# Performance work log

Measured on AMD Instinct MI355X. Metric: run time of the kernel, lower is better.

Reference implementation:

```python
import jax, jax.numpy as jnp
import numpy as np

N = 50000          # nodes
E = 800000         # edges
H = 64             # hidden_dim == node_embedding_dim (heads=1)
ED = 32            # edge_embedding_dim
L = 3              # num_layers - 1 TransformerConv layers
G = 256            # graphs in batch
NODE_CAT = 42
EDGE_CAT = 10
OUT = 32
SCALE = 1.0 / np.sqrt(H)


def segment_softmax(logits, seg, num_segments):
    mx = jax.ops.segment_max(logits, seg, num_segments=num_segments)
    e = jnp.exp(logits - mx[seg])
    denom = jax.ops.segment_sum(e, seg, num_segments=num_segments)
    return e / denom[seg]


def setup_inputs() -> dict:
    key = jax.random.key(0)
    ks = jax.random.split(key, 16)

    def init(k, shape, fan_in):
        return (jax.random.normal(k, shape, jnp.float32) / np.sqrt(fan_in))

    inp = {}
    inp["x"] = jax.random.randint(ks[0], (N,), 0, NODE_CAT)
    inp["edge_index"] = jax.random.randint(ks[1], (2, E), 0, N)
    inp["edge_attr"] = jax.random.randint(ks[2], (E,), 0, EDGE_CAT)
    inp["batch"] = jnp.sort(jax.random.randint(ks[3], (N,), 0, G))

    inp["node_emb"] = init(ks[4], (NODE_CAT, H), 1)
    inp["edge_emb"] = init(ks[5], (EDGE_CAT, ED), 1)
    # stacked per-layer TransformerConv params (input dim is H for all layers
    # since node_embedding_dim == hidden_dim)
    inp["Wq"] = init(ks[6], (L, H, H), H)
    inp["Wk"] = init(ks[7], (L, H, H), H)
    inp["Wv"] = init(ks[8], (L, H, H), H)
    inp["We"] = init(ks[9], (L, ED, H), ED)   # lin_edge, bias=False in PyG
    inp["Wskip"] = init(ks[10], (L, H, H), H)
    inp["bq"] = jnp.zeros((L, H), jnp.float32)
    inp["bk"] = jnp.zeros((L, H), jnp.float32)
    inp["bv"] = jnp.zeros((L, H), jnp.float32)
    inp["bskip"] = jnp.zeros((L, H), jnp.float32)
    # attentional aggregation readout
    inp["gate_W"] = init(ks[11], (H, 1), H)
    inp["gate_b"] = jnp.zeros((1,), jnp.float32)
    inp["out_W"] = init(ks[12], (H, OUT), H)
    inp["out_b"] = jnp.zeros((OUT,), jnp.float32)
    return inp


def reference(x, edge_index, edge_attr, batch, node_emb, edge_emb,
              Wq, Wk, Wv, We, Wskip, bq, bk, bv, bskip,
              gate_W, gate_b, out_W, out_b):
    src, dst = edge_index[0], edge_index[1]
    h = node_emb[x]            # [N, H] node embedding lookup
    e_feat = edge_emb[edge_attr]  # [E, ED] edge embedding lookup

    for l in range(L):
        q = h @ Wq[l] + bq[l]          # [N, H]
        k = h @ Wk[l] + bk[l]
        v = h @ Wv[l] + bv[l]
        e = e_feat @ We[l]             # [E, H]
        k_j = k[src] + e               # key_j += lin_edge(edge_attr)
        alpha = jnp.sum(q[dst] * k_j, axis=-1) * SCALE   # [E]
        a = segment_softmax(alpha, dst, N)               # softmax over dst nbhd
        msg = (v[src] + e) * a[:, None]                  # [E, H]
        agg = jax.ops.segment_sum(msg, dst, num_segments=N)
        h = jax.nn.relu(agg + h @ Wskip[l] + bskip[l])   # root/skip + ReLU

    # AttentionalAggregation: gate = gate_nn(x); x = nn(x); softmax gate per graph
    gate = (h @ gate_W + gate_b)[:, 0]   # [N]
    y = h @ out_W + out_b                # [N, OUT]
    g = segment_softmax(gate, batch, G)  # [N]
    return jax.ops.segment_sum(g[:, None] * y, batch, num_segments=G)  # [G, OUT]
```

## Files before the change

### kernel.cpp

```cpp
#include <hip/hip_runtime.h>
#include <hip/hip_bf16.h>

#define N_NODES 50000
#define N_EDGES 800000
#define H 64
#define ED 32
#define LAYERS 3
#define NGRAPH 256
#define OUTD 32
#define SCALE 0.125f

#define BNODES 128
#define NBUCK 391
#define NB_HISTB 256
#define EPB (N_EDGES / NB_HISTB)

#define FB_HIST 256
#define FB_TE   8
#define FB_GB   2
#define FB_WB   192
#define FB_TAB  42
#define NB_FRONT (FB_HIST + FB_TE + FB_GB + FB_WB + FB_TAB)

#define NB_GATHER 3125
#define NB_SCAN   98
#define NB_AGG    3125

typedef __attribute__((ext_vector_type(8))) short bf16x8;
typedef __attribute__((ext_vector_type(4))) float f32x4;
typedef unsigned short ushort_t;

__device__ __forceinline__ unsigned f2bf(float f) {
    unsigned u = __float_as_uint(f);
    return (u + 0x7FFFu + ((u >> 16) & 1u)) >> 16;
}

__device__ __forceinline__ float radd16(float x) {
    x += __int_as_float(__builtin_amdgcn_update_dpp(0, __float_as_int(x), 0xB1, 0xF, 0xF, true));
    x += __int_as_float(__builtin_amdgcn_update_dpp(0, __float_as_int(x), 0x4E, 0xF, 0xF, true));
    x += __int_as_float(__builtin_amdgcn_update_dpp(0, __float_as_int(x), 0x124, 0xF, 0xF, true));
    x += __int_as_float(__builtin_amdgcn_update_dpp(0, __float_as_int(x), 0x128, 0xF, 0xF, true));
    return x;
}

__device__ __forceinline__ void build_bstart(const int* __restrict__ tot,
                                             int* bst, int* part, int t) {
    int u0 = t * 2, u1 = t * 2 + 1;
    int a0 = (u0 < NBUCK) ? tot[u0] : 0;
    int a1 = (u1 < NBUCK) ? tot[u1] : 0;
    part[t] = a0 + a1;
    __syncthreads();
    for (int off = 1; off < 256; off <<= 1) {
        int add = (t >= off) ? part[t - off] : 0;
        __syncthreads();
        part[t] += add;
        __syncthreads();
    }
    int excl = part[t] - (a0 + a1);
    if (u0 < NBUCK) bst[u0] = excl;
    if (u1 < NBUCK) bst[u1] = excl + a0;
    if (t == 0) bst[NBUCK] = N_EDGES;
    __syncthreads();
}

__global__ __launch_bounds__(256) void k_front(
    const int* __restrict__ x, const float* __restrict__ node_emb,
    const float* __restrict__ edge_emb, const float* __restrict__ We, float* __restrict__ te,
    const int* __restrict__ ei, int* __restrict__ hist,
    const int* __restrict__ batch, int* __restrict__ gs,
    const float* __restrict__ Wq, const float* __restrict__ Wk,
    const float* __restrict__ Wv, const float* __restrict__ Wsk,
    const float* __restrict__ bq, const float* __restrict__ bk,
    const float* __restrict__ bv, const float* __restrict__ bsk,
    ushort_t* __restrict__ wb16,
    unsigned* __restrict__ tqs, unsigned* __restrict__ tkv)
{
    __shared__ int lh[NBUCK];
    __shared__ float tb[4][64];
    int b = blockIdx.x, t = threadIdx.x;
    if (b < FB_HIST) {
        for (int i = t; i < NBUCK; i += 256) lh[i] = 0;
        __syncthreads();
        const int* dstp = ei + N_EDGES + b * EPB;
        for (int i = t; i < EPB; i += 256)
            atomicAdd(&lh[dstp[i] >> 7], 1);
        __syncthreads();
        for (int i = t; i < NBUCK; i += 256) hist[i * NB_HISTB + b] = lh[i];
    } else if (b < FB_HIST + FB_TE) {
        int i = (b - FB_HIST) * 256 + t;
        if (i < LAYERS * 10 * H) {
            int c = i & 63;
            int cat = (i >> 6) % 10;
            int l = i / (10 * H);
            float acc = 0.f;
            for (int d = 0; d < ED; d++)
                acc += edge_emb[cat * ED + d] * We[((size_t)l * ED + d) * H + c];
            te[i] = acc;
        }
    } else if (b < FB_HIST + FB_TE + FB_GB) {
        int g = (b - FB_HIST - FB_TE) * 256 + t;
        if (g <= NGRAPH) {
            int lo = 0, hi = N_NODES;
            while (lo < hi) {
                int mid = (lo + hi) >> 1;
                if (batch[mid] < g) lo = mid + 1; else hi = mid;
            }
            gs[g] = lo;
        }
    } else if (b < FB_HIST + FB_TE + FB_GB + FB_WB) {
        int g = (b - FB_HIST - FB_TE - FB_GB) * 256 + t;
        int l = g >> 14;
        int rem = g & 16383;
        int c_id = rem >> 11;
        int rr = (rem >> 3) & 255;
        int j = rem & 7;
        int mat = rr >> 6, n = rr & 63;
        int k = ((c_id >> 2) << 5) + ((c_id & 3) << 3) + j;
        const float* Wm = (mat == 0) ? Wq : (mat == 1) ? Wk : (mat == 2) ? Wv : Wsk;
        wb16[g] = (ushort_t)f2bf(Wm[(size_t)l * 4096 + k * 64 + n]);
    } else {
        int cat = b - (FB_HIST + FB_TE + FB_GB + FB_WB);
        int mat = t >> 6, c = t & 63;
        const float* Wm = (mat == 0) ? Wq : (mat == 1) ? Wk : (mat == 2) ? Wv : Wsk;
        const float* bm = (mat == 0) ? bq : (mat == 1) ? bk : (mat == 2) ? bv : bsk;
        float acc = bm[c];
        for (int k = 0; k < H; k++)
            acc += node_emb[cat * H + k] * Wm[k * 64 + c];
        tb[mat][c] = acc;
        __syncthreads();
        if (t < 64) {
            tqs[cat * 64 + t] = f2bf(tb[0][t]) | (f2bf(tb[3][t]) << 16);
            tkv[cat * 64 + t] = f2bf(tb[2][t]) | (f2bf(tb[1][t]) << 16);
        }
    }
}

__global__ __launch_bounds__(256) void k_scan_gather(
    const int* __restrict__ x,
    const unsigned* __restrict__ tqs, const unsigned* __restrict__ tkv,
    unsigned* __restrict__ qs_out, unsigned* __restrict__ kv_out,
    int* __restrict__ hist, int* __restrict__ tot)
{
    __shared__ int sv[256];
    int b = blockIdx.x, t = threadIdx.x;
    if (b < NB_GATHER) {
        int idx = b * 256 + t;
        int n = idx >> 4, c4 = idx & 15;
        int cat = x[n];
        ((uint4*)qs_out)[idx] = ((const uint4*)tqs)[cat * 16 + c4];
        ((uint4*)kv_out)[idx] = ((const uint4*)tkv)[cat * 16 + c4];
    } else {
        int sb = b - NB_GATHER;
        for (int r = 0; r < 4; r++) {
            int u = sb * 4 + r;
            if (u < NBUCK) {
                int v = hist[u * NB_HISTB + t];
                sv[t] = v;
                __syncthreads();
                for (int off = 1; off < 256; off <<= 1) {
                    int add = (t >= off) ? sv[t - off] : 0;
                    __syncthreads();
                    sv[t] += add;
                    __syncthreads();
                }
                int incl = sv[t];
                hist[u * NB_HISTB + t] = incl - v;
                if (t == 255) tot[u] = incl;
                __syncthreads();
            }
        }
    }
}

__global__ __launch_bounds__(256) void k_scatter(
    const int* __restrict__ ei, const int* __restrict__ ea,
    const int* __restrict__ hist, const int* __restrict__ tot,
    int* __restrict__ pmid)
{
    __shared__ int bst[NBUCK + 1];
    __shared__ int part[256];
    __shared__ int curS[NBUCK];
    int b = blockIdx.x, t = threadIdx.x;
    build_bstart(tot, bst, part, t);
    for (int u = t; u < NBUCK; u += 256)
        curS[u] = bst[u] + hist[u * NB_HISTB + b];
    __syncthreads();
    int e0 = b * EPB;
    for (int i = t; i < EPB; i += 256) {
        int e = e0 + i;
        int src = ei[e], dst = ei[N_EDGES + e], cat = ea[e];
        int pos = atomicAdd(&curS[dst >> 7], 1);
        pmid[pos] = src | (cat << 16) | ((dst & 127) << 20);
    }
}

__global__ __launch_bounds__(256) void k_final(
    const int* __restrict__ pmid, const int* __restrict__ tot,
    int* __restrict__ packed, int* __restrict__ row_start, int* __restrict__ row_end)
{
    __shared__ int bst[NBUCK + 1];
    __shared__ int part[256];
    __shared__ int cnt[BNODES];
    __shared__ int scan_s[BNODES];
    int b = blockIdx.x, t = threadIdx.x;
    build_bstart(tot, bst, part, t);
    int beg = bst[b], end = bst[b + 1];
    if (t < BNODES) cnt[t] = 0;
    __syncthreads();
    for (int e = beg + t; e < end; e += 256)
        atomicAdd(&cnt[(pmid[e] >> 20) & 127], 1);
    __syncthreads();
    if (t < BNODES) scan_s[t] = cnt[t];
    __syncthreads();
    for (int off = 1; off < BNODES; off <<= 1) {
        int add = (t >= off && t < BNODES) ? scan_s[t - off] : 0;
        __syncthreads();
        if (t < BNODES) scan_s[t] += add;
        __syncthreads();
    }
    if (t < BNODES) {
        int c = cnt[t];
        int excl = scan_s[t] - c;
        int node = b * BNODES + t;
        if (node < N_NODES) {
            row_start[node] = beg + excl;
            row_end[node] = beg + excl + c;
        }
        cnt[t] = beg + excl;
    }
    __syncthreads();
    for (int e = beg + t; e < end; e += 256) {
        int p = pmid[e];
        int pos = atomicAdd(&cnt[(p >> 20) & 127], 1);
        packed[pos] = p & 0xFFFFF;
    }
}

struct EdgeLd { uint4 kv; float4 t; };
__device__ __forceinline__ EdgeLd edge_load(int pkt, const unsigned* __restrict__ kv32,
                                            const float* tel, int i16) {
    EdgeLd r;
    r.kv = *(const uint4*)(kv32 + ((size_t)(pkt & 0xFFFF) << 6) + (i16 << 2));
    r.t  = *(const float4*)(tel + ((pkt >> 16) << 6) + (i16 << 2));
    return r;
}
__device__ __forceinline__ float edge_dot(const EdgeLd& e, const float4& q4) {
    float p;
    p = (__uint_as_float(e.kv.x & 0xFFFF0000u) + e.t.x) * q4.x;
    p = fmaf(__uint_as_float(e.kv.y & 0xFFFF0000u) + e.t.y, q4.y, p);
    p = fmaf(__uint_as_float(e.kv.z & 0xFFFF0000u) + e.t.z, q4.z, p);
    p = fmaf(__uint_as_float(e.kv.w & 0xFFFF0000u) + e.t.w, q4.w, p);
    return radd16(p) * SCALE;
}
__device__ __forceinline__ float4 edge_val(const EdgeLd& e) {
    float4 v;
    v.x = __uint_as_float(e.kv.x << 16) + e.t.x;
    v.y = __uint_as_float(e.kv.y << 16) + e.t.y;
    v.z = __uint_as_float(e.kv.z << 16) + e.t.z;
    v.w = __uint_as_float(e.kv.w << 16) + e.t.w;
    return v;
}

__global__ __launch_bounds__(256, 4) void k_agg(
    const int* __restrict__ row_start, const int* __restrict__ row_end,
    const int* __restrict__ packed,
    const unsigned* __restrict__ qs_in, const unsigned* __restrict__ kv_in,
    const float* __restrict__ te,
    const ushort_t* __restrict__ wbn, const float* __restrict__ bqn,
    const float* __restrict__ bkn, const float* __restrict__ bvn,
    const float* __restrict__ bsn,
    unsigned* __restrict__ qs_out, unsigned* __restrict__ kv_out,
    float* __restrict__ hf, const float* __restrict__ gW,
    const float* __restrict__ gb, float* __restrict__ gate)
{
    __shared__ float tel[10 * 64];
    __shared__ ushort_t hs16[16 * 64];
    int t = threadIdx.x;
    int wave = t >> 6, lane = t & 63;
    int g = lane >> 4, i16 = lane & 15;
    int dst = blockIdx.x * 16 + wave * 4 + g;
    int beg = row_start[dst];
    int end = row_end[dst];
    uint4 uq = *(const uint4*)(qs_in + (size_t)dst * 64 + (i16 << 2));
    for (int i = t; i < 10 * 64; i += 256) tel[i] = te[i];
    __syncthreads();
    float4 q4, s4;
    q4.x = __uint_as_float(uq.x << 16); s4.x = __uint_as_float(uq.x & 0xFFFF0000u);
    q4.y = __uint_as_float(uq.y << 16); s4.y = __uint_as_float(uq.y & 0xFFFF0000u);
    q4.z = __uint_as_float(uq.z << 16); s4.z = __uint_as_float(uq.z & 0xFFFF0000u);
    q4.w = __uint_as_float(uq.w << 16); s4.w = __uint_as_float(uq.w & 0xFFFF0000u);
    float m = -1e30f, l = 0.f;
    float4 acc = {0.f, 0.f, 0.f, 0.f};
    int e = beg;
    for (; e + 3 < end; e += 4) {
        int p0 = packed[e], p1 = packed[e + 1], p2 = packed[e + 2], p3 = packed[e + 3];
        EdgeLd e0 = edge_load(p0, kv_in, tel, i16);
        EdgeLd e1 = edge_load(p1, kv_in, tel, i16);
        EdgeLd e2 = edge_load(p2, kv_in, tel, i16);
        EdgeLd e3 = edge_load(p3, kv_in, tel, i16);
        float a0 = edge_dot(e0, q4), a1 = edge_dot(e1, q4);
        float a2 = edge_dot(e2, q4), a3 = edge_dot(e3, q4);
        float mn = fmaxf(m, fmaxf(fmaxf(a0, a1), fmaxf(a2, a3)));
        float corr = __expf(m - mn);
        float w0 = __expf(a0 - mn), w1 = __expf(a1 - mn);
        float w2 = __expf(a2 - mn), w3 = __expf(a3 - mn);
        float4 v0 = edge_val(e0), v1 = edge_val(e1), v2 = edge_val(e2), v3 = edge_val(e3);
        acc.x = fmaf(w0, v0.x, fmaf(w1, v1.x, fmaf(w2, v2.x, fmaf(w3, v3.x, acc.x * corr))));
        acc.y = fmaf(w0, v0.y, fmaf(w1, v1.y, fmaf(w2, v2.y, fmaf(w3, v3.y, acc.y * corr))));
        acc.z = fmaf(w0, v0.z, fmaf(w1, v1.z, fmaf(w2, v2.z, fmaf(w3, v3.z, acc.z * corr))));
        acc.w = fmaf(w0, v0.w, fmaf(w1, v1.w, fmaf(w2, v2.w, fmaf(w3, v3.w, acc.w * corr))));
        l = fmaf(l, corr, (w0 + w1) + (w2 + w3));
        m = mn;
    }
    for (; e < end; e++) {
        int pkt = packed[e];
        EdgeLd e0 = edge_load(pkt, kv_in, tel, i16);
        float a = edge_dot(e0, q4);
        float mn = fmaxf(m, a);
        float corr = __expf(m - mn);
        float w = __expf(a - mn);
        float4 v4 = edge_val(e0);
        acc.x = fmaf(w, v4.x, acc.x * corr);
        acc.y = fmaf(w, v4.y, acc.y * corr);
        acc.z = fmaf(w, v4.z, acc.z * corr);
        acc.w = fmaf(w, v4.w, acc.w * corr);
        l = fmaf(l, corr, w);
        m = mn;
    }
    float inv = (l > 0.f) ? 1.f / l : 0.f;
    float4 hv;
    hv.x = fmaxf(acc.x * inv + s4.x, 0.f);
    hv.y = fmaxf(acc.y * inv + s4.y, 0.f);
    hv.z = fmaxf(acc.z * inv + s4.z, 0.f);
    hv.w = fmaxf(acc.w * inv + s4.w, 0.f);
    if (hf) *(float4*)(hf + (size_t)dst * H + (i16 << 2)) = hv;
    if (gW) {
        float4 g4 = *(const float4*)(gW + (i16 << 2));
        float p = hv.x * g4.x + hv.y * g4.y + hv.z * g4.z + hv.w * g4.w;
        p = radd16(p);
        if (i16 == 0) gate[dst] = p + gb[0];
    }
    if (wbn) {
        uint2 hp;
        hp.x = f2bf(hv.x) | (f2bf(hv.y) << 16);
        hp.y = f2bf(hv.z) | (f2bf(hv.w) << 16);
        *(uint2*)(hs16 + (((wave * 4 + g) << 6) + (i16 << 2))) = hp;
        __syncthreads();
        int n16 = lane & 15, quad = lane >> 4;
        f32x4 oacc[4];
        #pragma unroll
        for (int i = 0; i < 4; i++) oacc[i] = (f32x4){0.f, 0.f, 0.f, 0.f};
        #pragma unroll
        for (int kb = 0; kb < 2; kb++) {
            bf16x8 afr = *(const bf16x8*)(hs16 + ((n16 << 6) + kb * 32 + quad * 8));
            #pragma unroll
            for (int mat = 0; mat < 4; mat++) {
                int ct = mat * 4 + wave;
                const bf16x8* bp = (const bf16x8*)(wbn + (((kb * 4 + quad) << 11) + ((ct * 16 + n16) << 3)));
                oacc[mat] = __builtin_amdgcn_mfma_f32_16x16x32_bf16(afr, *bp, oacc[mat], 0, 0, 0);
            }
        }
        int col = (wave << 4) + n16;
        float bQ = bqn[col], bK = bkn[col], bV = bvn[col], bS = bsn[col];
        int nb = blockIdx.x * 16 + quad * 4;
        #pragma unroll
        for (int r = 0; r < 4; r++) {
            qs_out[(size_t)(nb + r) * 64 + col] = f2bf(oacc[0][r] + bQ) | (f2bf(oacc[3][r] + bS) << 16);
            kv_out[(size_t)(nb + r) * 64 + col] = f2bf(oacc[2][r] + bV) | (f2bf(oacc[1][r] + bK) << 16);
        }
    }
}

__global__ __launch_bounds__(256) void k_readout2(
    const float* __restrict__ h, const float* __restrict__ oW,
    const float* __restrict__ ob, const float* __restrict__ gate,
    const int* __restrict__ gs, float* __restrict__ out)
{
    __shared__ float hs[8][H + 1];
    __shared__ float red[256];
    __shared__ float den_s[8];
    __shared__ float gmax_s, den_tot;
    int t = threadIdx.x;
    int g = blockIdx.x;
    int ln = t >> 5, o = t & 31;
    float wreg[H];
    #pragma unroll
    for (int i = 0; i < H; i++) wreg[i] = oW[i * OUTD + o];
    int beg = gs[g], end = gs[g + 1];
    float mx = -INFINITY;
    for (int n = beg + t; n < end; n += 256) mx = fmaxf(mx, gate[n]);
    red[t] = mx;
    __syncthreads();
    for (int sft = 128; sft > 0; sft >>= 1) {
        if (t < sft) red[t] = fmaxf(red[t], red[t + sft]);
        __syncthreads();
    }
    if (t == 0) gmax_s = red[0];
    __syncthreads();
    float gm = gmax_s;
    float acc = 0.f, den = 0.f;
    for (int n0 = beg; n0 < end; n0 += 8) {
        __syncthreads();
        for (int i = t; i < 8 * H; i += 256) {
            int r = i >> 6, c = i & 63;
            int n = n0 + r;
            hs[r][c] = (n < end) ? h[(size_t)n * H + c] : 0.f;
        }
        __syncthreads();
        int n = n0 + ln;
        if (n < end) {
            float wt = __expf(gate[n] - gm);
            float d0 = 0.f;
            #pragma unroll
            for (int i = 0; i < H; i++) d0 += hs[ln][i] * wreg[i];
            acc += wt * d0;
            if (o == 0) den += wt;
        }
    }
    __syncthreads();
    red[t] = acc;
    if (o == 0) den_s[ln] = den;
    __syncthreads();
    for (int sft = 4; sft >= 1; sft >>= 1) {
        if (ln < sft) red[t] += red[t + sft * 32];
        __syncthreads();
    }
    if (t == 0) {
        float dt = 0.f;
        #pragma unroll
        for (int i = 0; i < 8; i++) dt += den_s[i];
        den_tot = dt;
    }
    __syncthreads();
    if (ln == 0) {
        float dt = den_tot;
        out[g * OUTD + o] = (dt > 0.f) ? red[o] / dt + ob[o] : 0.f;
    }
}

extern "C" void kernel_launch(void* const* d_in, const int* in_sizes, int n_in,
                              void* d_out, int out_size, void* d_ws, size_t ws_size,
                              hipStream_t stream)
{
    const int* x        = (const int*)d_in[0];
    const int* ei       = (const int*)d_in[1];
    const int* ea       = (const int*)d_in[2];
    const int* batch    = (const int*)d_in[3];
    const float* node_emb = (const float*)d_in[4];
    const float* edge_emb = (const float*)d_in[5];
    const float* Wq    = (const float*)d_in[6];
    const float* Wk    = (const float*)d_in[7];
    const float* Wv    = (const float*)d_in[8];
    const float* We    = (const float*)d_in[9];
    const float* Wskip = (const float*)d_in[10];
    const float* bq    = (const float*)d_in[11];
    const float* bk    = (const float*)d_in[12];
    const float* bv    = (const float*)d_in[13];
    const float* bskip = (const float*)d_in[14];
    const float* gate_W = (const float*)d_in[15];
    const float* gate_b = (const float*)d_in[16];
    const float* out_W  = (const float*)d_in[17];
    const float* out_b  = (const float*)d_in[18];
    float* out = (float*)d_out;

    const size_t NH = (size_t)N_NODES * H;
    float* ws   = (float*)d_ws;
    unsigned* qs_a = (unsigned*)ws;
    unsigned* kv_a = qs_a + NH;
    unsigned* qs_b = kv_a + NH;
    unsigned* kv_b = qs_b + NH;
    float* hf32 = (float*)(kv_b + NH);
    float* te   = hf32 + NH;
    float* gate = te + LAYERS * 10 * H;
    int* row_start = (int*)(gate + N_NODES);
    int* row_end   = row_start + N_NODES;
    int* packed    = row_end + N_NODES;
    int* pmid      = packed + N_EDGES;
    int* hist      = pmid + N_EDGES;
    int* tot       = hist + NBUCK * NB_HISTB;
    int* gs        = tot + NBUCK;
    unsigned* tqs  = (unsigned*)(gs + NGRAPH + 1);
    unsigned* tkv  = tqs + FB_TAB * 64;
    ushort_t* wb16 = (ushort_t*)(tkv + FB_TAB * 64);

    k_front<<<NB_FRONT, 256, 0, stream>>>(x, node_emb, edge_emb, We, te, ei, hist, batch, gs,
                                          Wq, Wk, Wv, Wskip, bq, bk, bv, bskip, wb16, tqs, tkv);
    k_scan_gather<<<NB_GATHER + NB_SCAN, 256, 0, stream>>>(x, tqs, tkv, qs_a, kv_a, hist, tot);
    k_scatter<<<NB_HISTB, 256, 0, stream>>>(ei, ea, hist, tot, pmid);
    k_final<<<NBUCK, 256, 0, stream>>>(pmid, tot, packed, row_start, row_end);

    k_agg<<<NB_AGG, 256, 0, stream>>>(
        row_start, row_end, packed, qs_a, kv_a, te,
        wb16 + (size_t)1 * 16384, bq + H, bk + H, bv + H, bskip + H, qs_b, kv_b,
        nullptr, nullptr, nullptr, nullptr);
    k_agg<<<NB_AGG, 256, 0, stream>>>(
        row_start, row_end, packed, qs_b, kv_b, te + 10 * H,
        wb16 + (size_t)2 * 16384, bq + 2 * H, bk + 2 * H, bv + 2 * H, bskip + 2 * H, qs_a, kv_a,
        nullptr, nullptr, nullptr, nullptr);
    k_agg<<<NB_AGG, 256, 0, stream>>>(
        row_start, row_end, packed, qs_a, kv_a, te + 2 * 10 * H,
        nullptr, nullptr, nullptr, nullptr, nullptr, nullptr, nullptr,
        hf32, gate_W, gate_b, gate);

    k_readout2<<<NGRAPH, 256, 0, stream>>>(hf32, out_W, out_b, gate, gs, out);
}
```

Before: 269.9 us.

## Fuse layer-0 node gather into aggregation via per-category LDS tables and packed edge keys

Removes the separate layer-0 node-feature gather pass. The edge packet now encodes the combined source node category and edge category, so the first aggregation kernel reads the per-category key/value table from LDS instead of per-node global rows. All aggregation kernels also stage each block's edge packets into LDS when they fit, and the kernels are specialized by template mode to drop runtime null checks. The cost is an extra x[src] lookup in the scatter and more LDS per block in the first layer, which may reduce occupancy.

```diff
diff --git a/kernel.cpp b/kernel.cpp
--- a/kernel.cpp
+++ b/kernel.cpp
@@ -9,6 +9,7 @@
 #define NGRAPH 256
 #define OUTD 32
 #define SCALE 0.125f
+#define NCAT 42
 
 #define BNODES 128
 #define NBUCK 391
@@ -19,12 +20,12 @@
 #define FB_TE   8
 #define FB_GB   2
 #define FB_WB   192
-#define FB_TAB  42
+#define FB_TAB  NCAT
 #define NB_FRONT (FB_HIST + FB_TE + FB_GB + FB_WB + FB_TAB)
 
-#define NB_GATHER 3125
 #define NB_SCAN   98
 #define NB_AGG    3125
+#define PKCAP     768
 
 typedef __attribute__((ext_vector_type(8))) short bf16x8;
 typedef __attribute__((ext_vector_type(4))) float f32x4;
@@ -135,45 +136,32 @@
     }
 }
 
-__global__ __launch_bounds__(256) void k_scan_gather(
-    const int* __restrict__ x,
-    const unsigned* __restrict__ tqs, const unsigned* __restrict__ tkv,
-    unsigned* __restrict__ qs_out, unsigned* __restrict__ kv_out,
-    int* __restrict__ hist, int* __restrict__ tot)
+__global__ __launch_bounds__(256) void k_scan(int* __restrict__ hist, int* __restrict__ tot)
 {
     __shared__ int sv[256];
-    int b = blockIdx.x, t = threadIdx.x;
-    if (b < NB_GATHER) {
-        int idx = b * 256 + t;
-        int n = idx >> 4, c4 = idx & 15;
-        int cat = x[n];
-        ((uint4*)qs_out)[idx] = ((const uint4*)tqs)[cat * 16 + c4];
-        ((uint4*)kv_out)[idx] = ((const uint4*)tkv)[cat * 16 + c4];
-    } else {
-        int sb = b - NB_GATHER;
-        for (int r = 0; r < 4; r++) {
-            int u = sb * 4 + r;
-            if (u < NBUCK) {
-                int v = hist[u * NB_HISTB + t];
-                sv[t] = v;
+    int sb = blockIdx.x, t = threadIdx.x;
+    for (int r = 0; r < 4; r++) {
+        int u = sb * 4 + r;
+        if (u < NBUCK) {
+            int v = hist[u * NB_HISTB + t];
+            sv[t] = v;
+            __syncthreads();
+            for (int off = 1; off < 256; off <<= 1) {
+                int add = (t >= off) ? sv[t - off] : 0;
                 __syncthreads();
-                for (int off = 1; off < 256; off <<= 1) {
-                    int add = (t >= off) ? sv[t - off] : 0;
-                    __syncthreads();
-                    sv[t] += add;
-                    __syncthreads();
-                }
-                int incl = sv[t];
-                hist[u * NB_HISTB + t] = incl - v;
-                if (t == 255) tot[u] = incl;
+                sv[t] += add;
                 __syncthreads();
             }
+            int incl = sv[t];
+            hist[u * NB_HISTB + t] = incl - v;
+            if (t == 255) tot[u] = incl;
+            __syncthreads();
         }
     }
 }
 
 __global__ __launch_bounds__(256) void k_scatter(
-    const int* __restrict__ ei, const int* __restrict__ ea,
+    const int* __restrict__ ei, const int* __restrict__ ea, const int* __restrict__ x,
     const int* __restrict__ hist, const int* __restrict__ tot,
     int* __restrict__ pmid)
 {
@@ -189,8 +177,9 @@
     for (int i = t; i < EPB; i += 256) {
         int e = e0 + i;
         int src = ei[e], dst = ei[N_EDGES + e], cat = ea[e];
+        int xs = x[src];
         int pos = atomicAdd(&curS[dst >> 7], 1);
-        pmid[pos] = src | (cat << 16) | ((dst & 127) << 20);
+        pmid[pos] = src | ((cat * NCAT + xs) << 16) | ((dst & 127) << 25);
     }
 }
 
@@ -208,7 +197,7 @@
     if (t < BNODES) cnt[t] = 0;
     __syncthreads();
     for (int e = beg + t; e < end; e += 256)
-        atomicAdd(&cnt[(pmid[e] >> 20) & 127], 1);
+        atomicAdd(&cnt[((unsigned)pmid[e] >> 25) & 127], 1);
     __syncthreads();
     if (t < BNODES) scan_s[t] = cnt[t];
     __syncthreads();
@@ -231,19 +220,12 @@
     __syncthreads();
     for (int e = beg + t; e < end; e += 256) {
         int p = pmid[e];
-        int pos = atomicAdd(&cnt[(p >> 20) & 127], 1);
-        packed[pos] = p & 0xFFFFF;
+        int pos = atomicAdd(&cnt[((unsigned)p >> 25) & 127], 1);
+        packed[pos] = p & 0x1FFFFFF;
     }
 }
 
 struct EdgeLd { uint4 kv; float4 t; };
-__device__ __forceinline__ EdgeLd edge_load(int pkt, const unsigned* __restrict__ kv32,
-                                            const float* tel, int i16) {
-    EdgeLd r;
-    r.kv = *(const uint4*)(kv32 + ((size_t)(pkt & 0xFFFF) << 6) + (i16 << 2));
-    r.t  = *(const float4*)(tel + ((pkt >> 16) << 6) + (i16 << 2));
-    return r;
-}
 __device__ __forceinline__ float edge_dot(const EdgeLd& e, const float4& q4) {
     float p;
     p = (__uint_as_float(e.kv.x & 0xFFFF0000u) + e.t.x) * q4.x;
@@ -261,29 +243,42 @@
     return v;
 }
 
-__global__ __launch_bounds__(256, 4) void k_agg(
+template<int MODE>
+__device__ __forceinline__ void agg_body(
     const int* __restrict__ row_start, const int* __restrict__ row_end,
-    const int* __restrict__ packed,
+    const int* __restrict__ packed, const int* __restrict__ x,
     const unsigned* __restrict__ qs_in, const unsigned* __restrict__ kv_in,
+    const unsigned* __restrict__ tqs, const unsigned* __restrict__ tkv,
     const float* __restrict__ te,
     const ushort_t* __restrict__ wbn, const float* __restrict__ bqn,
     const float* __restrict__ bkn, const float* __restrict__ bvn,
     const float* __restrict__ bsn,
     unsigned* __restrict__ qs_out, unsigned* __restrict__ kv_out,
     float* __restrict__ hf, const float* __restrict__ gW,
-    const float* __restrict__ gb, float* __restrict__ gate)
-{
-    __shared__ float tel[10 * 64];
-    __shared__ ushort_t hs16[16 * 64];
-    int t = threadIdx.x;
+    const float* __restrict__ gb, float* __restrict__ gate,
+    float* tel, unsigned* tqsl, unsigned* tkvl, ushort_t* hs16, int* pkl)
+{
+    int t = threadIdx.x, bid = blockIdx.x;
     int wave = t >> 6, lane = t & 63;
     int g = lane >> 4, i16 = lane & 15;
-    int dst = blockIdx.x * 16 + wave * 4 + g;
-    int beg = row_start[dst];
-    int end = row_end[dst];
-    uint4 uq = *(const uint4*)(qs_in + (size_t)dst * 64 + (i16 << 2));
-    for (int i = t; i < 10 * 64; i += 256) tel[i] = te[i];
-    __syncthreads();
+    int dst = bid * 16 + wave * 4 + g;
+    int beg = row_start[dst], end = row_end[dst];
+    int beg0 = row_start[bid * 16];
+    int cnt = row_end[bid * 16 + 15] - beg0;
+    bool use_lds = (cnt <= PKCAP);
+    for (int i = t; i < 640; i += 256) tel[i] = te[i];
+    if constexpr (MODE == 0) {
+        for (int i = t; i < NCAT * 64; i += 256) { tqsl[i] = tqs[i]; tkvl[i] = tkv[i]; }
+    }
+    if (use_lds) for (int i = t; i < cnt; i += 256) pkl[i] = packed[beg0 + i];
+    uint4 uq = {0u, 0u, 0u, 0u};
+    if constexpr (MODE != 0)
+        uq = *(const uint4*)(qs_in + (size_t)dst * 64 + (i16 << 2));
+    __syncthreads();
+    if constexpr (MODE == 0) {
+        int xd = x[dst];
+        uq = *(const uint4*)(tqsl + (xd << 6) + (i16 << 2));
+    }
     float4 q4, s4;
     q4.x = __uint_as_float(uq.x << 16); s4.x = __uint_as_float(uq.x & 0xFFFF0000u);
     q4.y = __uint_as_float(uq.y << 16); s4.y = __uint_as_float(uq.y & 0xFFFF0000u);
@@ -291,56 +286,71 @@
     q4.w = __uint_as_float(uq.w << 16); s4.w = __uint_as_float(uq.w & 0xFFFF0000u);
     float m = -1e30f, l = 0.f;
     float4 acc = {0.f, 0.f, 0.f, 0.f};
-    int e = beg;
-    for (; e + 3 < end; e += 4) {
-        int p0 = packed[e], p1 = packed[e + 1], p2 = packed[e + 2], p3 = packed[e + 3];
-        EdgeLd e0 = edge_load(p0, kv_in, tel, i16);
-        EdgeLd e1 = edge_load(p1, kv_in, tel, i16);
-        EdgeLd e2 = edge_load(p2, kv_in, tel, i16);
-        EdgeLd e3 = edge_load(p3, kv_in, tel, i16);
-        float a0 = edge_dot(e0, q4), a1 = edge_dot(e1, q4);
-        float a2 = edge_dot(e2, q4), a3 = edge_dot(e3, q4);
-        float mn = fmaxf(m, fmaxf(fmaxf(a0, a1), fmaxf(a2, a3)));
-        float corr = __expf(m - mn);
-        float w0 = __expf(a0 - mn), w1 = __expf(a1 - mn);
-        float w2 = __expf(a2 - mn), w3 = __expf(a3 - mn);
-        float4 v0 = edge_val(e0), v1 = edge_val(e1), v2 = edge_val(e2), v3 = edge_val(e3);
-        acc.x = fmaf(w0, v0.x, fmaf(w1, v1.x, fmaf(w2, v2.x, fmaf(w3, v3.x, acc.x * corr))));
-        acc.y = fmaf(w0, v0.y, fmaf(w1, v1.y, fmaf(w2, v2.y, fmaf(w3, v3.y, acc.y * corr))));
-        acc.z = fmaf(w0, v0.z, fmaf(w1, v1.z, fmaf(w2, v2.z, fmaf(w3, v3.z, acc.z * corr))));
-        acc.w = fmaf(w0, v0.w, fmaf(w1, v1.w, fmaf(w2, v2.w, fmaf(w3, v3.w, acc.w * corr))));
-        l = fmaf(l, corr, (w0 + w1) + (w2 + w3));
-        m = mn;
-    }
-    for (; e < end; e++) {
-        int pkt = packed[e];
-        EdgeLd e0 = edge_load(pkt, kv_in, tel, i16);
-        float a = edge_dot(e0, q4);
-        float mn = fmaxf(m, a);
-        float corr = __expf(m - mn);
-        float w = __expf(a - mn);
-        float4 v4 = edge_val(e0);
-        acc.x = fmaf(w, v4.x, acc.x * corr);
-        acc.y = fmaf(w, v4.y, acc.y * corr);
-        acc.z = fmaf(w, v4.z, acc.z * corr);
-        acc.w = fmaf(w, v4.w, acc.w * corr);
-        l = fmaf(l, corr, w);
-        m = mn;
-    }
+
+    auto eload = [&](int pkt) {
+        EdgeLd r;
+        unsigned catx = ((unsigned)pkt >> 16) & 0x1FFu;
+        int cat = (int)((catx * 1561u) >> 16);
+        r.t = *(const float4*)(tel + (cat << 6) + (i16 << 2));
+        if constexpr (MODE == 0) {
+            int xc = (int)catx - cat * NCAT;
+            r.kv = *(const uint4*)(tkvl + (xc << 6) + (i16 << 2));
+        } else {
+            int src = pkt & 0xFFFF;
+            r.kv = *(const uint4*)(kv_in + ((size_t)src << 6) + (i16 << 2));
+        }
+        return r;
+    };
+    auto run = [&](auto PKT) {
+        int e = beg;
+        for (; e + 3 < end; e += 4) {
+            int p0 = PKT(e), p1 = PKT(e + 1), p2 = PKT(e + 2), p3 = PKT(e + 3);
+            EdgeLd e0 = eload(p0), e1 = eload(p1), e2 = eload(p2), e3 = eload(p3);
+            float a0 = edge_dot(e0, q4), a1 = edge_dot(e1, q4);
+            float a2 = edge_dot(e2, q4), a3 = edge_dot(e3, q4);
+            float mn = fmaxf(m, fmaxf(fmaxf(a0, a1), fmaxf(a2, a3)));
+            float corr = __expf(m - mn);
+            float w0 = __expf(a0 - mn), w1 = __expf(a1 - mn);
+            float w2 = __expf(a2 - mn), w3 = __expf(a3 - mn);
+            float4 v0 = edge_val(e0), v1 = edge_val(e1), v2 = edge_val(e2), v3 = edge_val(e3);
+            acc.x = fmaf(w0, v0.x, fmaf(w1, v1.x, fmaf(w2, v2.x, fmaf(w3, v3.x, acc.x * corr))));
+            acc.y = fmaf(w0, v0.y, fmaf(w1, v1.y, fmaf(w2, v2.y, fmaf(w3, v3.y, acc.y * corr))));
+            acc.z = fmaf(w0, v0.z, fmaf(w1, v1.z, fmaf(w2, v2.z, fmaf(w3, v3.z, acc.z * corr))));
+            acc.w = fmaf(w0, v0.w, fmaf(w1, v1.w, fmaf(w2, v2.w, fmaf(w3, v3.w, acc.w * corr))));
+            l = fmaf(l, corr, (w0 + w1) + (w2 + w3));
+            m = mn;
+        }
+        for (; e < end; e++) {
+            EdgeLd e0 = eload(PKT(e));
+            float a = edge_dot(e0, q4);
+            float mn = fmaxf(m, a);
+            float corr = __expf(m - mn);
+            float w = __expf(a - mn);
+            float4 v4 = edge_val(e0);
+            acc.x = fmaf(w, v4.x, acc.x * corr);
+            acc.y = fmaf(w, v4.y, acc.y * corr);
+            acc.z = fmaf(w, v4.z, acc.z * corr);
+            acc.w = fmaf(w, v4.w, acc.w * corr);
+            l = fmaf(l, corr, w);
+            m = mn;
+        }
+    };
+    if (use_lds) run([&](int e) { return pkl[e - beg0]; });
+    else         run([&](int e) { return packed[e]; });
+
     float inv = (l > 0.f) ? 1.f / l : 0.f;
     float4 hv;
     hv.x = fmaxf(acc.x * inv + s4.x, 0.f);
     hv.y = fmaxf(acc.y * inv + s4.y, 0.f);
     hv.z = fmaxf(acc.z * inv + s4.z, 0.f);
     hv.w = fmaxf(acc.w * inv + s4.w, 0.f);
-    if (hf) *(float4*)(hf + (size_t)dst * H + (i16 << 2)) = hv;
-    if (gW) {
+    if constexpr (MODE == 2) {
+        *(float4*)(hf + (size_t)dst * H + (i16 << 2)) = hv;
         float4 g4 = *(const float4*)(gW + (i16 << 2));
         float p = hv.x * g4.x + hv.y * g4.y + hv.z * g4.z + hv.w * g4.w;
         p = radd16(p);
         if (i16 == 0) gate[dst] = p + gb[0];
-    }
-    if (wbn) {
+    } else {
         uint2 hp;
         hp.x = f2bf(hv.x) | (f2bf(hv.y) << 16);
         hp.y = f2bf(hv.z) | (f2bf(hv.w) << 16);
@@ -362,13 +372,66 @@
         }
         int col = (wave << 4) + n16;
         float bQ = bqn[col], bK = bkn[col], bV = bvn[col], bS = bsn[col];
-        int nb = blockIdx.x * 16 + quad * 4;
+        int nb = bid * 16 + quad * 4;
         #pragma unroll
         for (int r = 0; r < 4; r++) {
             qs_out[(size_t)(nb + r) * 64 + col] = f2bf(oacc[0][r] + bQ) | (f2bf(oacc[3][r] + bS) << 16);
             kv_out[(size_t)(nb + r) * 64 + col] = f2bf(oacc[2][r] + bV) | (f2bf(oacc[1][r] + bK) << 16);
         }
     }
+}
+
+__global__ __launch_bounds__(256, 4) void k_agg0(
+    const int* __restrict__ row_start, const int* __restrict__ row_end,
+    const int* __restrict__ packed, const int* __restrict__ x,
+    const unsigned* __restrict__ tqs, const unsigned* __restrict__ tkv,
+    const float* __restrict__ te,
+    const ushort_t* __restrict__ wbn, const float* __restrict__ bqn,
+    const float* __restrict__ bkn, const float* __restrict__ bvn,
+    const float* __restrict__ bsn,
+    unsigned* __restrict__ qs_out, unsigned* __restrict__ kv_out)
+{
+    __shared__ float tel[640];
+    __shared__ unsigned tqsl[NCAT * 64];
+    __shared__ unsigned tkvl[NCAT * 64];
+    __shared__ ushort_t hs16[1024];
+    __shared__ int pkl[PKCAP];
+    agg_body<0>(row_start, row_end, packed, x, nullptr, nullptr, tqs, tkv, te,
+                wbn, bqn, bkn, bvn, bsn, qs_out, kv_out,
+                nullptr, nullptr, nullptr, nullptr, tel, tqsl, tkvl, hs16, pkl);
+}
+
+__global__ __launch_bounds__(256, 4) void k_agg1(
+    const int* __restrict__ row_start, const int* __restrict__ row_end,
+    const int* __restrict__ packed,
+    const unsigned* __restrict__ qs_in, const unsigned* __restrict__ kv_in,
+    const float* __restrict__ te,
+    const ushort_t* __restrict__ wbn, const float* __restrict__ bqn,
+    const float* __restrict__ bkn, const float* __restrict__ bvn,
+    const float* __restrict__ bsn,
+    unsigned* __restrict__ qs_out, unsigned* __restrict__ kv_out)
+{
+    __shared__ float tel[640];
+    __shared__ ushort_t hs16[1024];
+    __shared__ int pkl[PKCAP];
+    agg_body<1>(row_start, row_end, packed, nullptr, qs_in, kv_in, nullptr, nullptr, te,
+                wbn, bqn, bkn, bvn, bsn, qs_out, kv_out,
+                nullptr, nullptr, nullptr, nullptr, tel, nullptr, nullptr, hs16, pkl);
+}
+
+__global__ __launch_bounds__(256, 4) void k_agg2(
+    const int* __restrict__ row_start, const int* __restrict__ row_end,
+    const int* __restrict__ packed,
+    const unsigned* __restrict__ qs_in, const unsigned* __restrict__ kv_in,
+    const float* __restrict__ te,
+    float* __restrict__ hf, const float* __restrict__ gW,
+    const float* __restrict__ gb, float* __restrict__ gate)
+{
+    __shared__ float tel[640];
+    __shared__ int pkl[PKCAP];
+    agg_body<2>(row_start, row_end, packed, nullptr, qs_in, kv_in, nullptr, nullptr, te,
+                nullptr, nullptr, nullptr, nullptr, nullptr, nullptr, nullptr,
+                hf, gW, gb, gate, tel, nullptr, nullptr, nullptr, pkl);
 }
 
 __global__ __launch_bounds__(256) void k_readout2(
@@ -485,21 +548,18 @@
 
     k_front<<<NB_FRONT, 256, 0, stream>>>(x, node_emb, edge_emb, We, te, ei, hist, batch, gs,
                                           Wq, Wk, Wv, Wskip, bq, bk, bv, bskip, wb16, tqs, tkv);
-    k_scan_gather<<<NB_GATHER + NB_SCAN, 256, 0, stream>>>(x, tqs, tkv, qs_a, kv_a, hist, tot);
-    k_scatter<<<NB_HISTB, 256, 0, stream>>>(ei, ea, hist, tot, pmid);
+    k_scan<<<NB_SCAN, 256, 0, stream>>>(hist, tot);
+    k_scatter<<<NB_HISTB, 256, 0, stream>>>(ei, ea, x, hist, tot, pmid);
     k_final<<<NBUCK, 256, 0, stream>>>(pmid, tot, packed, row_start, row_end);
 
-    k_agg<<<NB_AGG, 256, 0, stream>>>(
-        row_start, row_end, packed, qs_a, kv_a, te,
-        wb16 + (size_t)1 * 16384, bq + H, bk + H, bv + H, bskip + H, qs_b, kv_b,
-        nullptr, nullptr, nullptr, nullptr);
-    k_agg<<<NB_AGG, 256, 0, stream>>>(
-        row_start, row_end, packed, qs_b, kv_b, te + 10 * H,
-        wb16 + (size_t)2 * 16384, bq + 2 * H, bk + 2 * H, bv + 2 * H, bskip + 2 * H, qs_a, kv_a,
-        nullptr, nullptr, nullptr, nullptr);
-    k_agg<<<NB_AGG, 256, 0, stream>>>(
-        row_start, row_end, packed, qs_a, kv_a, te + 2 * 10 * H,
-        nullptr, nullptr, nullptr, nullptr, nullptr, nullptr, nullptr,
+    k_agg0<<<NB_AGG, 256, 0, stream>>>(
+        row_start, row_end, packed, x, tqs, tkv, te,
+        wb16 + (size_t)1 * 16384, bq + H, bk + H, bv + H, bskip + H, qs_a, kv_a);
+    k_agg1<<<NB_AGG, 256, 0, stream>>>(
+        row_start, row_end, packed, qs_a, kv_a, te + 10 * H,
+        wb16 + (size_t)2 * 16384, bq + 2 * H, bk + 2 * H, bv + 2 * H, bskip + 2 * H, qs_b, kv_b);
+    k_agg2<<<NB_AGG, 256, 0, stream>>>(
+        row_start, row_end, packed, qs_b, kv_b, te + 2 * 10 * H,
         hf32, gate_W, gate_b, gate);
 
     k_readout2<<<NGRAPH, 256, 0, stream>>>(hf32, out_W, out_b, gate, gs, out);
```

After: 262.1 us. 1.03x faster.
